# Kernel optimization log

Measured on AMD Instinct MI355X. Metric: run time of the kernel, lower is better.

Reference implementation:

```python
import jax, jax.numpy as jnp
import numpy as np

N = 100000   # nodes
E = 1600000  # edges
IN = 64
HID = 64
C = 2
EPS = 1e-12


def _linear_init(k, fan_in, fan_out):
    s = 1.0 / np.sqrt(fan_in)
    kw, kb = jax.random.split(k)
    w = jax.random.uniform(kw, (fan_in, fan_out), minval=-s, maxval=s, dtype=jnp.float32)
    b = jax.random.uniform(kb, (fan_out,), minval=-s, maxval=s, dtype=jnp.float32)
    return w, b


def setup_inputs() -> dict:
    key = jax.random.key(0)
    ks = jax.random.split(key, 12)
    x = jax.random.normal(ks[0], (N, IN), dtype=jnp.float32)
    edge_index = jax.random.randint(ks[1], (2, E), 0, N, dtype=jnp.int64)
    w1, b1 = _linear_init(ks[2], IN, HID)
    w2, b2 = _linear_init(ks[3], HID, HID)
    w3, b3 = _linear_init(ks[4], HID, HID)
    wg1, bg1 = _linear_init(ks[5], HID, HID)   # GCNConv 1
    wg2, bg2 = _linear_init(ks[6], HID, HID)   # GCNConv 2
    beta = jnp.ones((), dtype=jnp.float32)     # AGNN learnable scalar
    wf, bf = _linear_init(ks[7], HID, HID)     # W_f
    wx, bx = _linear_init(ks[8], HID, HID)     # W_x
    wc, bc = _linear_init(ks[9], 2 * HID, C)   # classifier
    return {"x": x, "edge_index": edge_index,
            "w1": w1, "b1": b1, "w2": w2, "b2": b2, "w3": w3, "b3": b3,
            "wg1": wg1, "bg1": bg1, "wg2": wg2, "bg2": bg2, "beta": beta,
            "wf": wf, "bf": bf, "wx": wx, "bx": bx, "wc": wc, "bc": bc}


def _segment_softmax(logits, seg, n):
    m = jax.ops.segment_max(logits, seg, num_segments=n)
    e = jnp.exp(logits - m[seg])
    s = jax.ops.segment_sum(e, seg, num_segments=n)
    return e / s[seg]


def _gcn_conv(x, w, b, row, col, norm):
    # x' = D^{-1/2}(A+I)D^{-1/2} x W + b  (PyG GCNConv with self-loops)
    h = x @ w                                   # [N, HID]
    msg = h[row] * norm[:, None]                # gather + scale  [E+N, HID]
    out = jax.ops.segment_sum(msg, col, num_segments=N)
    return out + b


def _agnn_conv(x, beta, row, col):
    # cosine-similarity attention (PyG AGNNConv), self-loops included
    xn = x / (jnp.linalg.norm(x, axis=-1, keepdims=True) + EPS)
    alpha = beta * jnp.sum(xn[row] * xn[col], axis=-1)   # [E+N]
    a = _segment_softmax(alpha, col, N)
    return jax.ops.segment_sum(a[:, None] * x[row], col, num_segments=N)


def reference(x, edge_index, w1, b1, w2, b2, w3, b3, wg1, bg1, wg2, bg2,
              beta, wf, bf, wx, bx, wc, bc):
    # add self-loops
    loop = jnp.arange(N, dtype=edge_index.dtype)
    row = jnp.concatenate([edge_index[0], loop])
    col = jnp.concatenate([edge_index[1], loop])
    # symmetric GCN normalization
    deg = jax.ops.segment_sum(jnp.ones_like(col, dtype=jnp.float32), col, num_segments=N)
    dinv = jnp.where(deg > 0, deg ** -0.5, 0.0)
    norm = dinv[row] * dinv[col]

    # input MLP
    h = jax.nn.relu(x @ w1 + b1)
    h = jax.nn.relu(h @ w2 + b2)
    h = h @ w3 + b3                              # [N, HID]

    f0 = _gcn_conv(h, wg1, bg1, row, col, norm)
    f1 = _gcn_conv(h, wg2, bg2, row, col, norm)
    h1 = _agnn_conv(h, beta, row, col)

    h_filters = jnp.stack([f0, f1], axis=1)      # [N, 2, HID]
    h_proj = jnp.tanh(h_filters @ wf + bf)       # [N, 2, HID]
    x_proj = jnp.tanh(h @ wx + bx)               # [N, HID]
    logit = jnp.einsum('nkh,nh->nk', h_proj, x_proj)   # bmm -> [N, 2]
    score = jax.nn.softmax(logit, axis=1)
    res = jnp.einsum('nkh,nk->nh', h_filters, score)   # attention-weighted fusion
    res = jnp.concatenate([res, h1], axis=1)     # [N, 2*HID]
    y_hat = res @ wc + bc                        # dropout disabled (eval)
    return y_hat
```

## Files before the change

kernel.cpp:

```cpp
#include <hip/hip_runtime.h>
#include <math.h>


#define SCT 8192

typedef float v2f __attribute__((ext_vector_type(2)));

__device__ __forceinline__ v2f v2fma(v2f a, v2f b, v2f c) {
#if __has_builtin(__builtin_elementwise_fma)
    return __builtin_elementwise_fma(a, b, c);
#else
    v2f r; r.x = fmaf(a.x, b.x, c.x); r.y = fmaf(a.y, b.y, c.y); return r;
#endif
}

__device__ __forceinline__ void lds_fence() {
    asm volatile("s_waitcnt lgkmcnt(0)" ::: "memory");
}

__device__ __forceinline__ float fast_tanh(float x) {
    x = fminf(fmaxf(x, -15.f), 15.f);
    float e = __expf(2.f * x);
    return (e - 1.f) * __frcp_rn(e + 1.f);
}

__device__ __forceinline__ void fma4(float (&acc)[4], float a, const float4& w) {
    acc[0] = fmaf(a, w.x, acc[0]);
    acc[1] = fmaf(a, w.y, acc[1]);
    acc[2] = fmaf(a, w.z, acc[2]);
    acc[3] = fmaf(a, w.w, acc[3]);
}

__device__ __forceinline__ void load_rows32(const float* __restrict__ src, int row0, int n,
                                            float (*dst)[68], int t)
{
    int e = t * 8;
    int r = e >> 6, i = e & 63;
    int grow = row0 + r;
    float4 v0 = make_float4(0.f, 0.f, 0.f, 0.f), v1 = v0;
    if (grow < n) {
        const float* p = src + (size_t)grow * 64 + i;
        v0 = *(const float4*)p;
        v1 = *(const float4*)(p + 4);
    }
    *(float4*)&dst[r][i]     = v0;
    *(float4*)&dst[r][i + 4] = v1;
}

__device__ __forceinline__ void gemm_core(const float (*in)[68], const float* w,
                                          const float* b, int rg, int cg,
                                          float (&acc0)[4], float (&acc1)[4])
{
#pragma unroll
    for (int dc = 0; dc < 4; dc++) { float bb = b[4*cg + dc]; acc0[dc] = bb; acc1[dc] = bb; }
    const int r0 = 2 * rg, r1 = 2 * rg + 1;
#pragma unroll
    for (int i = 0; i < 64; i += 4) {
        float4 a0 = *(const float4*)&in[r0][i];
        float4 a1 = *(const float4*)&in[r1][i];
        float4 q0 = *(const float4*)&w[(i + 0) * 64 + 4 * cg];
        float4 q1 = *(const float4*)&w[(i + 1) * 64 + 4 * cg];
        float4 q2 = *(const float4*)&w[(i + 2) * 64 + 4 * cg];
        float4 q3 = *(const float4*)&w[(i + 3) * 64 + 4 * cg];
        fma4(acc0, a0.x, q0); fma4(acc0, a0.y, q1); fma4(acc0, a0.z, q2); fma4(acc0, a0.w, q3);
        fma4(acc1, a1.x, q0); fma4(acc1, a1.y, q1); fma4(acc1, a1.z, q2); fma4(acc1, a1.w, q3);
    }
}

__device__ __forceinline__ void gemm4_gw(const float (*in)[68], const float* __restrict__ w,
                                         const float* b, int rgs, int cg,
                                         float (&acc)[4][4])
{
#pragma unroll
    for (int r = 0; r < 4; r++) {
#pragma unroll
        for (int dc = 0; dc < 4; dc++) acc[r][dc] = b[4 * cg + dc];
    }
    const float* wp = w + 4 * cg;
    const int r0 = 4 * rgs;
#pragma unroll 2
    for (int i = 0; i < 64; i += 4) {
        float4 q0 = *(const float4*)&wp[(i + 0) * 64];
        float4 q1 = *(const float4*)&wp[(i + 1) * 64];
        float4 q2 = *(const float4*)&wp[(i + 2) * 64];
        float4 q3 = *(const float4*)&wp[(i + 3) * 64];
#pragma unroll
        for (int r = 0; r < 4; r++) {
            float4 a = *(const float4*)&in[r0 + r][i];
            fma4(acc[r], a.x, q0); fma4(acc[r], a.y, q1);
            fma4(acc[r], a.z, q2); fma4(acc[r], a.w, q3);
        }
    }
}


__global__ __launch_bounds__(256) void k_zero(int* __restrict__ arr, int n1)
{
    int i = blockIdx.x * 256 + threadIdx.x;
    if (i < n1) arr[i] = 0;
}

__global__ __launch_bounds__(256) void k_bhist(const int* __restrict__ col,
                                               int* __restrict__ bhist, int e)
{
    __shared__ int hist[256];
    int t = threadIdx.x;
    hist[t] = 0;
    __syncthreads();
    int base = blockIdx.x * SCT;
    int end = min(e, base + SCT);
    for (int i = base + t; i < end; i += 256)
        atomicAdd(&hist[col[i] >> 9], 1);
    __syncthreads();
    if (hist[t]) atomicAdd(&bhist[t], hist[t]);
}

__global__ __launch_bounds__(256) void k_bscan(const int* __restrict__ bhist,
                                               int* __restrict__ bbase, int* __restrict__ bcur)
{
    __shared__ int s[256];
    int t = threadIdx.x;
    int v = bhist[t];
    s[t] = v;
    __syncthreads();
    for (int d = 1; d < 256; d <<= 1) {
        int u = (t >= d) ? s[t - d] : 0;
        __syncthreads();
        s[t] += u;
        __syncthreads();
    }
    int b = s[t] - v;
    bbase[t] = b;
    bcur[t] = b;
}

__global__ __launch_bounds__(256) void k_bscatter2(const int* __restrict__ row,
    const int* __restrict__ col, int* __restrict__ bcur,
    int2* __restrict__ pairs, int e, int nbk)
{
    __shared__ int hist[256], lcur[256], gb[256], s[256];
    __shared__ int2 buf[SCT];
    int t = threadIdx.x;
    int base = blockIdx.x * SCT;
    int end = min(e, base + SCT);
    hist[t] = 0;
    __syncthreads();
    for (int i = base + t; i < end; i += 256)
        atomicAdd(&hist[col[i] >> 9], 1);
    __syncthreads();
    int v = hist[t];
    s[t] = v;
    __syncthreads();
    for (int d = 1; d < 256; d <<= 1) {
        int u = (t >= d) ? s[t - d] : 0;
        __syncthreads();
        s[t] += u;
        __syncthreads();
    }
    lcur[t] = s[t] - v;
    __syncthreads();
    for (int i = base + t; i < end; i += 256) {
        int c = col[i];
        int slot = atomicAdd(&lcur[c >> 9], 1);
        buf[slot] = make_int2(row[i], c);
    }
    if (v > 0) gb[t] = atomicAdd(&bcur[t], v);
    __syncthreads();
    for (int b = 0; b < nbk; b++) {
        int cnt = hist[b];
        if (cnt == 0) continue;
        int lo = s[b] - cnt;
        int go = gb[b];
        for (int j = t; j < cnt; j += 256)
            pairs[go + j] = buf[lo + j];
    }
}

__global__ __launch_bounds__(256) void k_fill3(const int2* __restrict__ pairs,
    const int* __restrict__ bbase, const int* __restrict__ bhist,
    int* __restrict__ arr, int* __restrict__ csr, int n)
{
    __shared__ int nh[512], nc[512], s[256];
    int b = blockIdx.x, t = threadIdx.x;
    int pbase = bbase[b];
    int cnt = bhist[b];
    int nodebase = b << 9;
    nh[t] = 0; nh[t + 256] = 0;
    __syncthreads();
    for (int i = t; i < cnt; i += 256)
        atomicAdd(&nh[pairs[pbase + i].y - nodebase], 1);
    __syncthreads();
    int v0 = nh[2 * t], v1 = nh[2 * t + 1];
    int sum = v0 + v1;
    s[t] = sum;
    __syncthreads();
    for (int d = 1; d < 256; d <<= 1) {
        int u = (t >= d) ? s[t - d] : 0;
        __syncthreads();
        s[t] += u;
        __syncthreads();
    }
    int excl = s[t] - sum;
    int n0 = nodebase + 2 * t, n1 = n0 + 1;
    nc[2 * t]     = pbase + excl;
    nc[2 * t + 1] = pbase + excl + v0;
    if (n0 < n) arr[n0] = pbase + excl + v0;
    if (n1 < n) arr[n1] = pbase + excl + v0 + v1;
    __syncthreads();
    for (int i = t; i < cnt; i += 256) {
        int2 pr = pairs[pbase + i];
        int p = atomicAdd(&nc[pr.y - nodebase], 1);
        csr[p] = pr.x;
    }
}


__global__ __launch_bounds__(256) void k_pre(
    const float* __restrict__ wg1, const float* __restrict__ bg1,
    const float* __restrict__ wg2, const float* __restrict__ bg2,
    const float* __restrict__ wf,  const float* __restrict__ bf,
    const float* __restrict__ wc,  float* __restrict__ pre)
{
    __shared__ float wfs[4096];
    __shared__ float wcs[128];
    int t = threadIdx.x;
    for (int i = t; i < 4096; i += 256) wfs[i] = wf[i];
    if (t < 128) wcs[t] = wc[t];
    __syncthreads();
    int i = t & 63, jb = (t >> 6) * 16;
    float acc0[16], acc1[16];
#pragma unroll
    for (int j = 0; j < 16; j++) { acc0[j] = 0.f; acc1[j] = 0.f; }
#pragma unroll 1
    for (int k = 0; k < 64; k++) {
        float a = wg1[i * 64 + k];
        float b = wg2[i * 64 + k];
#pragma unroll
        for (int j = 0; j < 16; j++) {
            float w = wfs[k * 64 + jb + j];
            acc0[j] = fmaf(a, w, acc0[j]);
            acc1[j] = fmaf(b, w, acc1[j]);
        }
    }
#pragma unroll
    for (int j = 0; j < 16; j++) {
        pre[i * 64 + jb + j]        = acc0[j];
        pre[4096 + i * 64 + jb + j] = acc1[j];
    }
    if (t < 64) {
        float s0 = bf[t], s1 = bf[t];
#pragma unroll 1
        for (int m = 0; m < 64; m++) {
            s0 = fmaf(bg1[m], wfs[m * 64 + t], s0);
            s1 = fmaf(bg2[m], wfs[m * 64 + t], s1);
        }
        pre[8192 + t] = s0;
        pre[8256 + t] = s1;
        float u00 = 0.f, u01 = 0.f, u10 = 0.f, u11 = 0.f;
#pragma unroll 1
        for (int m = 0; m < 64; m++) {
            float g1 = wg1[t * 64 + m], g2 = wg2[t * 64 + m];
            u00 = fmaf(g1, wcs[m * 2 + 0], u00);
            u01 = fmaf(g1, wcs[m * 2 + 1], u01);
            u10 = fmaf(g2, wcs[m * 2 + 0], u10);
            u11 = fmaf(g2, wcs[m * 2 + 1], u11);
        }
        pre[8320 + t * 2]     = u00;
        pre[8320 + t * 2 + 1] = u01;
        pre[8448 + t * 2]     = u10;
        pre[8448 + t * 2 + 1] = u11;
    }
    if (t == 0) {
        float v00 = 0.f, v01 = 0.f, v10 = 0.f, v11 = 0.f;
#pragma unroll 1
        for (int m = 0; m < 64; m++) {
            v00 = fmaf(bg1[m], wcs[m * 2 + 0], v00);
            v01 = fmaf(bg1[m], wcs[m * 2 + 1], v01);
            v10 = fmaf(bg2[m], wcs[m * 2 + 0], v10);
            v11 = fmaf(bg2[m], wcs[m * 2 + 1], v11);
        }
        pre[8576] = v00; pre[8577] = v01; pre[8578] = v10; pre[8579] = v11;
    }
}


__global__ __launch_bounds__(256) void k_mlp(const float* __restrict__ x,
    const float* __restrict__ w1, const float* __restrict__ b1,
    const float* __restrict__ w2, const float* __restrict__ b2,
    const float* __restrict__ w3, const float* __restrict__ b3,
    const int* __restrict__ arr, float* __restrict__ h,
    float2* __restrict__ nrm2, int n)
{
    __shared__ float b1s[64], b2s[64], b3s[64];
    __shared__ float xs[4][16][68];
    int t = threadIdx.x;
    if (t < 64) { b1s[t] = b1[t]; b2s[t] = b2[t]; b3s[t] = b3[t]; }
    __syncthreads();
    int wv = t >> 6, lane = t & 63;
    int cg = lane & 15, rgs = lane >> 4;
    int row0 = blockIdx.x * 64 + wv * 16;
    float (*ws)[68] = xs[wv];

    {
        int r = lane >> 2, c = (lane & 3) * 16;
        int grow = row0 + r;
        float4 v0 = make_float4(0.f,0.f,0.f,0.f), v1 = v0, v2 = v0, v3 = v0;
        if (grow < n) {
            const float* p = x + (size_t)grow * 64 + c;
            v0 = *(const float4*)p;       v1 = *(const float4*)(p + 4);
            v2 = *(const float4*)(p + 8); v3 = *(const float4*)(p + 12);
        }
        *(float4*)&ws[r][c]      = v0; *(float4*)&ws[r][c + 4]  = v1;
        *(float4*)&ws[r][c + 8]  = v2; *(float4*)&ws[r][c + 12] = v3;
    }
    lds_fence();

    float acc[4][4];
    gemm4_gw(ws, w1, b1s, rgs, cg, acc);
    lds_fence();
#pragma unroll
    for (int r = 0; r < 4; r++)
        *(float4*)&ws[4 * rgs + r][4 * cg] =
            make_float4(fmaxf(acc[r][0], 0.f), fmaxf(acc[r][1], 0.f),
                        fmaxf(acc[r][2], 0.f), fmaxf(acc[r][3], 0.f));
    lds_fence();
    gemm4_gw(ws, w2, b2s, rgs, cg, acc);
    lds_fence();
#pragma unroll
    for (int r = 0; r < 4; r++)
        *(float4*)&ws[4 * rgs + r][4 * cg] =
            make_float4(fmaxf(acc[r][0], 0.f), fmaxf(acc[r][1], 0.f),
                        fmaxf(acc[r][2], 0.f), fmaxf(acc[r][3], 0.f));
    lds_fence();
    gemm4_gw(ws, w3, b3s, rgs, cg, acc);

    int r0g = row0 + 4 * rgs;
    float sr[4];
#pragma unroll
    for (int r = 0; r < 4; r++) {
        int grow = r0g + r;
        if (grow < n)
            *(float4*)&h[(size_t)grow * 64 + 4 * cg] =
                make_float4(acc[r][0], acc[r][1], acc[r][2], acc[r][3]);
        sr[r] = acc[r][0]*acc[r][0] + acc[r][1]*acc[r][1]
              + acc[r][2]*acc[r][2] + acc[r][3]*acc[r][3];
    }
#pragma unroll
    for (int d = 1; d < 16; d <<= 1) {
#pragma unroll
        for (int r = 0; r < 4; r++) sr[r] += __shfl_xor(sr[r], d, 64);
    }
    if (cg == 0) {
#pragma unroll
        for (int r = 0; r < 4; r++) {
            int grow = r0g + r;
            if (grow < n) {
                int st = (grow == 0) ? 0 : arr[grow - 1];
                nrm2[grow] = make_float2(1.0f / (sqrtf(sr[r]) + 1e-12f),
                                         rsqrtf((float)(arr[grow] - st + 1)));
            }
        }
    }
}


__global__ __launch_bounds__(256) void k_gather(const float* __restrict__ h,
    const int* __restrict__ arr, const int* __restrict__ csr,
    const float2* __restrict__ nrm2, const float* __restrict__ beta_p,
    const float* __restrict__ wc,
    float* __restrict__ agg, float2* __restrict__ yp, int n)
{
    __shared__ float reda[4][8][64];
    __shared__ float redn[4][8][64];
    int wv = threadIdx.x >> 6;
    int node = blockIdx.x * 4 + wv;
    if (node >= n) return;
    int lane = threadIdx.x & 63;
    int g = lane >> 3, s = lane & 7;
    float beta = beta_p[0];
    const char* hb = (const char*)h;

    unsigned selfoff = ((unsigned)node << 8) + ((unsigned)s << 5);
    float4 hA = *(const float4*)(hb + selfoff);
    float4 hB = *(const float4*)(hb + selfoff + 16);
    v2f hc0 = {hA.x, hA.y}, hc1 = {hA.z, hA.w};
    v2f hc2 = {hB.x, hB.y}, hc3 = {hB.z, hB.w};

    v2f sv = hc0 * hc0;
    sv = v2fma(hc1, hc1, sv); sv = v2fma(hc2, hc2, sv); sv = v2fma(hc3, hc3, sv);
    float ss = sv.x + sv.y;
#pragma unroll
    for (int d = 1; d < 8; d <<= 1) ss += __shfl_xor(ss, d, 64);
    float2 ncv = nrm2[node];
    float rnc = ncv.x, dc = ncv.y;
    float brn = beta * rnc;
    float wself = __expf(brn * ss * rnc);

    v2f a0 = {0.f,0.f}, a1 = {0.f,0.f}, a2 = {0.f,0.f}, a3 = {0.f,0.f};
    v2f n0 = {0.f,0.f}, n1 = {0.f,0.f}, n2 = {0.f,0.f}, n3 = {0.f,0.f};
    float denom = 0.f;
    if (g == 0) {
        v2f dcv = {dc, dc}, wsv = {wself, wself};
        a0 = dcv * hc0; a1 = dcv * hc1; a2 = dcv * hc2; a3 = dcv * hc3;
        n0 = wsv * hc0; n1 = wsv * hc1; n2 = wsv * hc2; n3 = wsv * hc3;
        denom = wself;
    }

    int start = (node == 0) ? 0 : arr[node - 1];
    int end = arr[node];
#pragma unroll 1
    for (int k0 = start; k0 < end; k0 += 64) {
        int m = min(64, end - k0);
        int idx = 0; float rv = 0.f, dv = 0.f;
        if (lane < m) {
            idx = csr[k0 + lane];
            float2 nd = nrm2[idx];
            rv = nd.x; dv = nd.y;
        }
        int ei = __shfl(idx, g, 64);
        unsigned eoff = ((unsigned)ei << 8) + ((unsigned)s << 5);
        float4 cA = *(const float4*)(hb + eoff);
        float4 cB = *(const float4*)(hb + eoff + 16);
#pragma unroll 1
        for (int k = 0; k < m; k += 8) {
            float4 fA = cA, fB = cB;
            if (k + 8 < m) {
                int e2 = __shfl(idx, k + 8 + g, 64);
                unsigned off2 = ((unsigned)e2 << 8) + ((unsigned)s << 5);
                cA = *(const float4*)(hb + off2);
                cB = *(const float4*)(hb + off2 + 16);
            }
            float rnr = __shfl(rv, k + g, 64);
            float dvr = __shfl(dv, k + g, 64);
            v2f f0 = {fA.x, fA.y}, f1 = {fA.z, fA.w};
            v2f f2 = {fB.x, fB.y}, f3 = {fB.z, fB.w};
            v2f ps = f0 * hc0;
            ps = v2fma(f1, hc1, ps); ps = v2fma(f2, hc2, ps); ps = v2fma(f3, hc3, ps);
            float p = ps.x + ps.y;
#pragma unroll
            for (int d = 1; d < 8; d <<= 1) p += __shfl_xor(p, d, 64);
            bool act = (k + g) < m;
            float w   = act ? __expf(brn * p * rnr) : 0.f;
            float dve = act ? dvr : 0.f;
            v2f wsp = {w, w}, dsp = {dve, dve};
            a0 = v2fma(dsp, f0, a0); a1 = v2fma(dsp, f1, a1);
            a2 = v2fma(dsp, f2, a2); a3 = v2fma(dsp, f3, a3);
            n0 = v2fma(wsp, f0, n0); n1 = v2fma(wsp, f1, n1);
            n2 = v2fma(wsp, f2, n2); n3 = v2fma(wsp, f3, n3);
            denom += w;
        }
    }

    {
        float* wa = &reda[wv][g][8 * s];
        float* wn = &redn[wv][g][8 * s];
        *(float4*)wa       = make_float4(a0.x, a0.y, a1.x, a1.y);
        *(float4*)(wa + 4) = make_float4(a2.x, a2.y, a3.x, a3.y);
        *(float4*)wn       = make_float4(n0.x, n0.y, n1.x, n1.y);
        *(float4*)(wn + 4) = make_float4(n2.x, n2.y, n3.x, n3.y);
    }
    const float* ra = &reda[wv][0][lane];
    const float* rn = &redn[wv][0][lane];
    float asum, nsum;
    {
        float t0 = ra[0]   + ra[64],  t1 = ra[128] + ra[192];
        float t2 = ra[256] + ra[320], t3 = ra[384] + ra[448];
        asum = (t0 + t1) + (t2 + t3);
        float u0 = rn[0]   + rn[64],  u1 = rn[128] + rn[192];
        float u2 = rn[256] + rn[320], u3 = rn[384] + rn[448];
        nsum = (u0 + u1) + (u2 + u3);
    }
    agg[(size_t)node * 64 + lane] = dc * asum;

#pragma unroll
    for (int d = 8; d < 64; d <<= 1) denom += __shfl_xor(denom, d, 64);

    float2 wcv = *(const float2*)(wc + 128 + 2 * lane);
    float cx = nsum * wcv.x, cy = nsum * wcv.y;
#pragma unroll
    for (int d = 1; d < 64; d <<= 1) { cx += __shfl_xor(cx, d, 64); cy += __shfl_xor(cy, d, 64); }
    if (lane == 0) {
        float inv = 1.0f / denom;
        yp[node] = make_float2(cx * inv, cy * inv);
    }
}


__global__ __launch_bounds__(256) void k_epi(const float* __restrict__ agg,
    const float* __restrict__ hbuf, const float2* __restrict__ yp,
    const float* __restrict__ pre, const float* __restrict__ wx,
    const float* __restrict__ bx, const float* __restrict__ bc,
    float* __restrict__ y, int n, int ntiles)
{
    __shared__ float W0s[4096], W1s[4096], wxs[4096];
    __shared__ float c0s[64], c1s[64], bxs[64], us[256], vs[4], bcs[2];
    __shared__ float A[32][68], H[32][68];
    int t = threadIdx.x;
    for (int i = t; i < 4096; i += 256) { W0s[i] = pre[i]; W1s[i] = pre[4096 + i]; wxs[i] = wx[i]; }
    if (t < 64) { c0s[t] = pre[8192 + t]; c1s[t] = pre[8256 + t]; bxs[t] = bx[t]; }
    us[t] = pre[8320 + t];
    if (t < 4) vs[t] = pre[8576 + t];
    if (t < 2) bcs[t] = bc[t];
    __syncthreads();
    int cg = t & 15, rg = t >> 4;
    for (int tile = blockIdx.x; tile < ntiles; tile += gridDim.x) {
        int row0 = tile * 32;
        load_rows32(agg,  row0, n, A, t);
        load_rows32(hbuf, row0, n, H, t);
        __syncthreads();
        int r0g = row0 + 2 * rg, r1g = r0g + 1;
        float xp0[4], xp1[4];
        gemm_core(H, wxs, bxs, rg, cg, xp0, xp1);
#pragma unroll
        for (int j = 0; j < 4; j++) { xp0[j] = fast_tanh(xp0[j]); xp1[j] = fast_tanh(xp1[j]); }
        float a0[4], a1[4];
        gemm_core(A, W0s, c0s, rg, cg, a0, a1);
        float l00 = 0.f, l01 = 0.f;
#pragma unroll
        for (int j = 0; j < 4; j++) {
            l00 = fmaf(fast_tanh(a0[j]), xp0[j], l00);
            l01 = fmaf(fast_tanh(a1[j]), xp1[j], l01);
        }
        gemm_core(A, W1s, c1s, rg, cg, a0, a1);
        float l10 = 0.f, l11 = 0.f;
#pragma unroll
        for (int j = 0; j < 4; j++) {
            l10 = fmaf(fast_tanh(a0[j]), xp0[j], l10);
            l11 = fmaf(fast_tanh(a1[j]), xp1[j], l11);
        }
        float4 av0 = *(const float4*)&A[2 * rg][4 * cg];
        float4 av1 = *(const float4*)&A[2 * rg + 1][4 * cg];
        float za0=0.f, za1=0.f, zb0=0.f, zb1=0.f;
        float zc0=0.f, zc1=0.f, zd0=0.f, zd1=0.f;
#pragma unroll
        for (int j = 0; j < 4; j++) {
            int k = 4 * cg + j;
            float u0c0 = us[k * 2], u0c1 = us[k * 2 + 1];
            float u1c0 = us[128 + k * 2], u1c1 = us[128 + k * 2 + 1];
            float p0 = (&av0.x)[j], p1 = (&av1.x)[j];
            za0 = fmaf(p0, u0c0, za0); za1 = fmaf(p0, u0c1, za1);
            zb0 = fmaf(p0, u1c0, zb0); zb1 = fmaf(p0, u1c1, zb1);
            zc0 = fmaf(p1, u0c0, zc0); zc1 = fmaf(p1, u0c1, zc1);
            zd0 = fmaf(p1, u1c0, zd0); zd1 = fmaf(p1, u1c1, zd1);
        }
#pragma unroll
        for (int d = 1; d < 16; d <<= 1) {
            l00 += __shfl_xor(l00, d, 64); l01 += __shfl_xor(l01, d, 64);
            l10 += __shfl_xor(l10, d, 64); l11 += __shfl_xor(l11, d, 64);
            za0 += __shfl_xor(za0, d, 64); za1 += __shfl_xor(za1, d, 64);
            zb0 += __shfl_xor(zb0, d, 64); zb1 += __shfl_xor(zb1, d, 64);
            zc0 += __shfl_xor(zc0, d, 64); zc1 += __shfl_xor(zc1, d, 64);
            zd0 += __shfl_xor(zd0, d, 64); zd1 += __shfl_xor(zd1, d, 64);
        }
        if (cg == 0) {
            if (r0g < n) {
                float mx = fmaxf(l00, l10);
                float e0 = __expf(l00 - mx), e1 = __expf(l10 - mx);
                float inv = 1.0f / (e0 + e1);
                float s0 = e0 * inv, s1 = e1 * inv;
                float2 ypv = yp[r0g];
                float y0v = s0 * (za0 + vs[0]) + s1 * (zb0 + vs[2]) + ypv.x + bcs[0];
                float y1v = s0 * (za1 + vs[1]) + s1 * (zb1 + vs[3]) + ypv.y + bcs[1];
                *(float2*)&y[(size_t)r0g * 2] = make_float2(y0v, y1v);
            }
            if (r1g < n) {
                float mx = fmaxf(l01, l11);
                float e0 = __expf(l01 - mx), e1 = __expf(l11 - mx);
                float inv = 1.0f / (e0 + e1);
                float s0 = e0 * inv, s1 = e1 * inv;
                float2 ypv = yp[r1g];
                float y0v = s0 * (zc0 + vs[0]) + s1 * (zd0 + vs[2]) + ypv.x + bcs[0];
                float y1v = s0 * (zc1 + vs[1]) + s1 * (zd1 + vs[3]) + ypv.y + bcs[1];
                *(float2*)&y[(size_t)r1g * 2] = make_float2(y0v, y1v);
            }
        }
        __syncthreads();
    }
}

extern "C" void kernel_launch(void* const* d_in, const int* in_sizes, int n_in,
                              void* d_out, int out_size, void* d_ws, size_t ws_size,
                              hipStream_t stream)
{
    const float* x    = (const float*)d_in[0];
    const int*   ei   = (const int*)d_in[1];
    const float* w1   = (const float*)d_in[2];
    const float* b1   = (const float*)d_in[3];
    const float* w2   = (const float*)d_in[4];
    const float* b2   = (const float*)d_in[5];
    const float* w3   = (const float*)d_in[6];
    const float* b3   = (const float*)d_in[7];
    const float* wg1  = (const float*)d_in[8];
    const float* bg1  = (const float*)d_in[9];
    const float* wg2  = (const float*)d_in[10];
    const float* bg2  = (const float*)d_in[11];
    const float* beta = (const float*)d_in[12];
    const float* wf   = (const float*)d_in[13];
    const float* bf   = (const float*)d_in[14];
    const float* wx   = (const float*)d_in[15];
    const float* bx   = (const float*)d_in[16];
    const float* wc   = (const float*)d_in[17];
    const float* bc   = (const float*)d_in[18];
    float* y = (float*)d_out;

    int n = in_sizes[0] / 64;
    int e = in_sizes[1] / 2;
    const int* row = ei;
    const int* col = ei + e;

    char* p = (char*)d_ws;
    auto alloc = [&](size_t bytes) { char* q = p; p += (bytes + 255) & ~(size_t)255; return q; };
    float*  h    = (float*)alloc((size_t)n * 64 * 4);
    int*    csr  = (int*)alloc((size_t)e * 4);
    float2* nrm2 = (float2*)alloc((size_t)n * 8);
    int*    arr  = (int*)alloc((size_t)(n + 1) * 4);
    float2* yp   = (float2*)alloc((size_t)n * 8);
    float*  pre  = (float*)alloc(8704 * 4);
    int*    bhist = (int*)alloc(256 * 4);
    int*    bbase = (int*)alloc(256 * 4);
    int*    bcur  = (int*)alloc(256 * 4);

    int2* pairs = (int2*)h;
    float* agg = (float*)d_in[0];

    int ntiles = (n + 31) / 32;
    int ntile64 = (n + 63) / 64;
    int nbk = (n + 511) >> 9;
    int nsct = (e + SCT - 1) / SCT;

    k_pre<<<1, 256, 0, stream>>>(wg1, bg1, wg2, bg2, wf, bf, wc, pre);
    k_zero<<<1, 256, 0, stream>>>(bhist, 256);
    k_bhist<<<nsct, 256, 0, stream>>>(col, bhist, e);
    k_bscan<<<1, 256, 0, stream>>>(bhist, bbase, bcur);
    k_bscatter2<<<nsct, 256, 0, stream>>>(row, col, bcur, pairs, e, nbk);
    k_fill3<<<nbk, 256, 0, stream>>>(pairs, bbase, bhist, arr, csr, n);
    k_mlp<<<ntile64, 256, 0, stream>>>(x, w1, b1, w2, b2, w3, b3, arr, h, nrm2, n);
    k_gather<<<(n + 3) / 4, 256, 0, stream>>>(h, arr, csr, nrm2, beta, wc, agg, yp, n);
    k_epi<<<1024, 256, 0, stream>>>(agg, h, yp, pre, wx, bx, bc, y, n, ntiles);
}
```

Before: 401.4 us.

## Process two nodes per wavefront in gather kernel using half-wave groups

The neighbor-gather kernel now assigns two destination nodes per 64-lane wavefront, with each 32-lane half handling 4 edges at a time instead of 8. With an average degree of about 16, this is meant to cut idle lanes in each 64-edge chunk and reduce per-node loop overhead. The LDS reduction layout is padded, and the final reductions work on half-waves. The cost is less edge parallelism per node, which means more serial iterations for high-degree nodes.

```diff
diff --git a/kernel.cpp b/kernel.cpp
--- a/kernel.cpp
+++ b/kernel.cpp
@@ -370,17 +370,21 @@
     const float* __restrict__ wc,
     float* __restrict__ agg, float2* __restrict__ yp, int n)
 {
-    __shared__ float reda[4][8][64];
-    __shared__ float redn[4][8][64];
+    __shared__ float reda[4][4][2][66];
+    __shared__ float redn[4][4][2][66];
     int wv = threadIdx.x >> 6;
-    int node = blockIdx.x * 4 + wv;
-    if (node >= n) return;
     int lane = threadIdx.x & 63;
-    int g = lane >> 3, s = lane & 7;
+    int sub = lane >> 5;
+    int l32 = lane & 31;
+    int g = l32 >> 3, s = l32 & 7;
+    int base = sub << 5;
+    int node = blockIdx.x * 8 + wv * 2 + sub;
+    bool valid = node < n;
+    int nd = valid ? node : 0;
     float beta = beta_p[0];
     const char* hb = (const char*)h;
 
-    unsigned selfoff = ((unsigned)node << 8) + ((unsigned)s << 5);
+    unsigned selfoff = ((unsigned)nd << 8) + ((unsigned)s << 5);
     float4 hA = *(const float4*)(hb + selfoff);
     float4 hB = *(const float4*)(hb + selfoff + 16);
     v2f hc0 = {hA.x, hA.y}, hc1 = {hA.z, hA.w};
@@ -391,7 +395,7 @@
     float ss = sv.x + sv.y;
 #pragma unroll
     for (int d = 1; d < 8; d <<= 1) ss += __shfl_xor(ss, d, 64);
-    float2 ncv = nrm2[node];
+    float2 ncv = nrm2[nd];
     float rnc = ncv.x, dc = ncv.y;
     float brn = beta * rnc;
     float wself = __expf(brn * ss * rnc);
@@ -406,32 +410,32 @@
         denom = wself;
     }
 
-    int start = (node == 0) ? 0 : arr[node - 1];
-    int end = arr[node];
+    int start = (!valid || nd == 0) ? 0 : arr[nd - 1];
+    int end = valid ? arr[nd] : 0;
 #pragma unroll 1
-    for (int k0 = start; k0 < end; k0 += 64) {
-        int m = min(64, end - k0);
+    for (int k0 = start; k0 < end; k0 += 32) {
+        int m = min(32, end - k0);
         int idx = 0; float rv = 0.f, dv = 0.f;
-        if (lane < m) {
-            idx = csr[k0 + lane];
-            float2 nd = nrm2[idx];
-            rv = nd.x; dv = nd.y;
-        }
-        int ei = __shfl(idx, g, 64);
+        if (l32 < m) {
+            idx = csr[k0 + l32];
+            float2 ndv = nrm2[idx];
+            rv = ndv.x; dv = ndv.y;
+        }
+        int ei = __shfl(idx, base + g, 64);
         unsigned eoff = ((unsigned)ei << 8) + ((unsigned)s << 5);
         float4 cA = *(const float4*)(hb + eoff);
         float4 cB = *(const float4*)(hb + eoff + 16);
 #pragma unroll 1
-        for (int k = 0; k < m; k += 8) {
+        for (int k = 0; k < m; k += 4) {
             float4 fA = cA, fB = cB;
-            if (k + 8 < m) {
-                int e2 = __shfl(idx, k + 8 + g, 64);
+            if (k + 4 < m) {
+                int e2 = __shfl(idx, base + k + 4 + g, 64);
                 unsigned off2 = ((unsigned)e2 << 8) + ((unsigned)s << 5);
                 cA = *(const float4*)(hb + off2);
                 cB = *(const float4*)(hb + off2 + 16);
             }
-            float rnr = __shfl(rv, k + g, 64);
-            float dvr = __shfl(dv, k + g, 64);
+            float rnr = __shfl(rv, base + k + g, 64);
+            float dvr = __shfl(dv, base + k + g, 64);
             v2f f0 = {fA.x, fA.y}, f1 = {fA.z, fA.w};
             v2f f2 = {fB.x, fB.y}, f3 = {fB.z, fB.w};
             v2f ps = f0 * hc0;
@@ -452,34 +456,44 @@
     }
 
     {
-        float* wa = &reda[wv][g][8 * s];
-        float* wn = &redn[wv][g][8 * s];
+        float* wa = &reda[wv][g][sub][8 * s];
+        float* wn = &redn[wv][g][sub][8 * s];
         *(float4*)wa       = make_float4(a0.x, a0.y, a1.x, a1.y);
         *(float4*)(wa + 4) = make_float4(a2.x, a2.y, a3.x, a3.y);
         *(float4*)wn       = make_float4(n0.x, n0.y, n1.x, n1.y);
         *(float4*)(wn + 4) = make_float4(n2.x, n2.y, n3.x, n3.y);
     }
-    const float* ra = &reda[wv][0][lane];
-    const float* rn = &redn[wv][0][lane];
-    float asum, nsum;
+    lds_fence();
+    float a_lo, a_hi, n_lo, n_hi;
     {
-        float t0 = ra[0]   + ra[64],  t1 = ra[128] + ra[192];
-        float t2 = ra[256] + ra[320], t3 = ra[384] + ra[448];
-        asum = (t0 + t1) + (t2 + t3);
-        float u0 = rn[0]   + rn[64],  u1 = rn[128] + rn[192];
-        float u2 = rn[256] + rn[320], u3 = rn[384] + rn[448];
-        nsum = (u0 + u1) + (u2 + u3);
-    }
-    agg[(size_t)node * 64 + lane] = dc * asum;
-
-#pragma unroll
-    for (int d = 8; d < 64; d <<= 1) denom += __shfl_xor(denom, d, 64);
-
-    float2 wcv = *(const float2*)(wc + 128 + 2 * lane);
-    float cx = nsum * wcv.x, cy = nsum * wcv.y;
-#pragma unroll
-    for (int d = 1; d < 64; d <<= 1) { cx += __shfl_xor(cx, d, 64); cy += __shfl_xor(cy, d, 64); }
-    if (lane == 0) {
+        const float* r0p = &reda[wv][0][sub][0];
+        const float* r1p = &redn[wv][0][sub][0];
+        float t0 = r0p[l32]       + r0p[132 + l32];
+        float t1 = r0p[264 + l32] + r0p[396 + l32];
+        float t2 = r0p[l32 + 32]       + r0p[132 + l32 + 32];
+        float t3 = r0p[264 + l32 + 32] + r0p[396 + l32 + 32];
+        a_lo = t0 + t1; a_hi = t2 + t3;
+        float u0 = r1p[l32]       + r1p[132 + l32];
+        float u1 = r1p[264 + l32] + r1p[396 + l32];
+        float u2 = r1p[l32 + 32]       + r1p[132 + l32 + 32];
+        float u3 = r1p[264 + l32 + 32] + r1p[396 + l32 + 32];
+        n_lo = u0 + u1; n_hi = u2 + u3;
+    }
+    if (valid) {
+        agg[(size_t)node * 64 + l32]      = dc * a_lo;
+        agg[(size_t)node * 64 + l32 + 32] = dc * a_hi;
+    }
+
+    denom += __shfl_xor(denom, 8, 64);
+    denom += __shfl_xor(denom, 16, 64);
+
+    float2 w_lo = *(const float2*)(wc + 128 + 2 * l32);
+    float2 w_hi = *(const float2*)(wc + 128 + 2 * (l32 + 32));
+    float cx = n_lo * w_lo.x + n_hi * w_hi.x;
+    float cy = n_lo * w_lo.y + n_hi * w_hi.y;
+#pragma unroll
+    for (int d = 1; d < 32; d <<= 1) { cx += __shfl_xor(cx, d, 64); cy += __shfl_xor(cy, d, 64); }
+    if (l32 == 0 && valid) {
         float inv = 1.0f / denom;
         yp[node] = make_float2(cx * inv, cy * inv);
     }
@@ -635,6 +649,6 @@
     k_bscatter2<<<nsct, 256, 0, stream>>>(row, col, bcur, pairs, e, nbk);
     k_fill3<<<nbk, 256, 0, stream>>>(pairs, bbase, bhist, arr, csr, n);
     k_mlp<<<ntile64, 256, 0, stream>>>(x, w1, b1, w2, b2, w3, b3, arr, h, nrm2, n);
-    k_gather<<<(n + 3) / 4, 256, 0, stream>>>(h, arr, csr, nrm2, beta, wc, agg, yp, n);
+    k_gather<<<(n + 7) / 8, 256, 0, stream>>>(h, arr, csr, nrm2, beta, wc, agg, yp, n);
     k_epi<<<1024, 256, 0, stream>>>(agg, h, yp, pre, wx, bx, bc, y, n, ntiles);
 }
```

After: 401.1 us. No clear change (-0.1%).
